# Kernel optimization log

Hardware: AMD Instinct MI355X
Metric: run time of the kernel (lower is better)

## Reference

```python
import jax, jax.numpy as jnp
import numpy as np

N_NODES = 40000
N_EDGES = 640000
D = 128
D_OUT = 128


def _layernorm(x, gamma, beta, eps=1e-5):
    mu = jnp.mean(x, axis=-1, keepdims=True)
    var = jnp.mean(jnp.square(x - mu), axis=-1, keepdims=True)
    return (x - mu) * jax.lax.rsqrt(var + eps) * gamma + beta


def setup_inputs() -> dict:
    key = jax.random.key(0)
    ks = jax.random.split(key, 6)
    x = jax.random.normal(ks[0], (N_NODES, D), dtype=jnp.float32)
    edge_index = jax.random.randint(ks[1], (2, N_EDGES), 0, N_NODES, dtype=jnp.int64)
    s = 1.0 / np.sqrt(D)
    return {
        "x": x,
        "edge_index": edge_index,
        "ln1_w": jnp.ones((D,), jnp.float32),
        "ln1_b": jnp.zeros((D,), jnp.float32),
        "ln2_w": jnp.ones((D,), jnp.float32),
        "ln2_b": jnp.zeros((D,), jnp.float32),
        "w": jnp.ones((D,), jnp.float32),
        "W1": jax.random.normal(ks[2], (D, D), jnp.float32) * s,
        "W2": jax.random.normal(ks[3], (D, D), jnp.float32) * s,
        "O1": jax.random.normal(ks[4], (2 * D, D), jnp.float32) * s,
        "O2": jax.random.normal(ks[5], (D, D_OUT), jnp.float32) * s,
    }


def reference(x, edge_index, ln1_w, ln1_b, ln2_w, ln2_b, w, W1, W2, O1, O2):
    row, col = edge_index[0], edge_index[1]
    n = x.shape[0]
    # gather + 2-layer message MLP (bias-free): [E, D]
    msg = jnp.maximum(x[row] @ W1, 0.0) @ W2
    # scatter_mean over destination nodes (zero where no incoming edges)
    agg = jax.ops.segment_sum(msg, col, num_segments=n)
    cnt = jax.ops.segment_sum(jnp.ones((msg.shape[0],), x.dtype), col, num_segments=n)
    agg = agg / jnp.maximum(cnt, 1.0)[:, None]
    agg_n = _layernorm(agg, ln1_w, ln1_b)
    # repulsion + residual + LayerNorm
    fx = _layernorm(x + (x - agg_n) * w, ln2_w, ln2_b)
    # concat + output MLP
    cat = jnp.concatenate([fx, agg_n], axis=1)
    return jnp.maximum(cat @ O1, 0.0) @ O2
```

## Files before the change

### kernel.cpp

```cpp
#include <hip/hip_runtime.h>
#include <hip/hip_bf16.h>

#define NN 40000
#define NE 640000
#define DD 128
#define CAP 64

typedef __attribute__((ext_vector_type(8))) short bf16x8;
typedef __attribute__((ext_vector_type(8))) unsigned short u16x8;
typedef __attribute__((ext_vector_type(4))) float f32x4;

__device__ __forceinline__ unsigned short f2bf(float f) {
    __hip_bfloat16 h = __float2bfloat16(f);
    return *reinterpret_cast<unsigned short*>(&h);
}
__device__ __forceinline__ float bf2f(unsigned short u) {
    union { unsigned int ui; float f; } v;
    v.ui = ((unsigned int)u) << 16;
    return v.f;
}

__global__ __launch_bounds__(256) void prep_w_kernel(
    const float* __restrict__ W1, const float* __restrict__ W2,
    const float* __restrict__ O1, const float* __restrict__ O2,
    unsigned short* __restrict__ w1t, unsigned short* __restrict__ w2t,
    unsigned short* __restrict__ o1t, unsigned short* __restrict__ o2t)
{
    int t = blockIdx.x * 256 + threadIdx.x;
    if (t < 16384) {
        int n = t >> 7, k = t & 127;
        w1t[t] = f2bf(W1[k * 128 + n]);
    } else if (t < 32768) {
        int i = t - 16384;
        int n = i >> 7, k = i & 127;
        w2t[i] = f2bf(W2[k * 128 + n]);
    } else if (t < 65536) {
        int i = t - 32768;
        int n = i >> 8, k = i & 255;
        o1t[i] = f2bf(O1[k * 128 + n]);
    } else {
        int i = t - 65536;
        int n = i >> 7, k = i & 127;
        o2t[i] = f2bf(O2[k * 128 + n]);
    }
}

__global__ __launch_bounds__(256) void mlp1_kernel(
    const float* __restrict__ x, const unsigned short* __restrict__ w1t,
    const unsigned short* __restrict__ w2t, unsigned short* __restrict__ nm)
{
    __shared__ unsigned short xt[64 * 128];
    __shared__ unsigned short wb[128 * 128];
    __shared__ unsigned short hb[64 * 128];
    const int tid = threadIdx.x;
    const int row0 = blockIdx.x * 64;

    #pragma unroll
    for (int it = 0; it < 4; ++it) {
        int c = tid + it * 256;
        int r = c >> 4;
        int c0 = (c & 15) << 3;
        const float4* gp = reinterpret_cast<const float4*>(x + (size_t)(row0 + r) * DD + c0);
        float4 f0 = gp[0], f1 = gp[1];
        u16x8 p;
        p[0] = f2bf(f0.x); p[1] = f2bf(f0.y); p[2] = f2bf(f0.z); p[3] = f2bf(f0.w);
        p[4] = f2bf(f1.x); p[5] = f2bf(f1.y); p[6] = f2bf(f1.z); p[7] = f2bf(f1.w);
        unsigned b = (unsigned)((r * DD + c0) * 2) ^ ((unsigned)(r & 7) << 4);
        *reinterpret_cast<u16x8*>(reinterpret_cast<char*>(xt) + b) = p;
    }
    #pragma unroll
    for (int it = 0; it < 8; ++it) {
        int c = tid + it * 256;
        int n = c >> 4;
        int k0 = (c & 15) << 3;
        u16x8 v = *reinterpret_cast<const u16x8*>(w1t + n * DD + k0);
        unsigned b = (unsigned)((n * DD + k0) * 2) ^ ((unsigned)(n & 7) << 4);
        *reinterpret_cast<u16x8*>(reinterpret_cast<char*>(wb) + b) = v;
    }
    __syncthreads();

    const int lane = tid & 63;
    const int wv = tid >> 6;
    const int l15 = lane & 15;
    const int lg = lane >> 4;

    f32x4 acc[8];
    #pragma unroll
    for (int i = 0; i < 8; ++i) acc[i] = (f32x4){0.f, 0.f, 0.f, 0.f};

    #pragma unroll
    for (int kk = 0; kk < 4; ++kk) {
        int k = kk * 32 + lg * 8;
        int ar = wv * 16 + l15;
        bf16x8 a = *reinterpret_cast<const bf16x8*>(
            reinterpret_cast<const char*>(xt) + ((unsigned)((ar * DD + k) * 2) ^ ((unsigned)(ar & 7) << 4)));
        #pragma unroll
        for (int n0 = 0; n0 < 8; ++n0) {
            int bn = n0 * 16 + l15;
            bf16x8 bf = *reinterpret_cast<const bf16x8*>(
                reinterpret_cast<const char*>(wb) + ((unsigned)((bn * DD + k) * 2) ^ ((unsigned)(bn & 7) << 4)));
            acc[n0] = __builtin_amdgcn_mfma_f32_16x16x32_bf16(a, bf, acc[n0], 0, 0, 0);
        }
    }

    #pragma unroll
    for (int n0 = 0; n0 < 8; ++n0) {
        #pragma unroll
        for (int ri = 0; ri < 4; ++ri) {
            int r = wv * 16 + lg * 4 + ri;
            int cc = n0 * 16 + l15;
            float v = fmaxf(acc[n0][ri], 0.0f);
            *reinterpret_cast<unsigned short*>(
                reinterpret_cast<char*>(hb) + ((unsigned)((r * DD + cc) * 2) ^ ((unsigned)(r & 7) << 4))) = f2bf(v);
        }
    }
    __syncthreads();
    #pragma unroll
    for (int it = 0; it < 8; ++it) {
        int c = tid + it * 256;
        int n = c >> 4;
        int k0 = (c & 15) << 3;
        u16x8 v = *reinterpret_cast<const u16x8*>(w2t + n * DD + k0);
        unsigned b = (unsigned)((n * DD + k0) * 2) ^ ((unsigned)(n & 7) << 4);
        *reinterpret_cast<u16x8*>(reinterpret_cast<char*>(wb) + b) = v;
    }
    __syncthreads();

    f32x4 acc2[8];
    #pragma unroll
    for (int i = 0; i < 8; ++i) acc2[i] = (f32x4){0.f, 0.f, 0.f, 0.f};
    #pragma unroll
    for (int kk = 0; kk < 4; ++kk) {
        int k = kk * 32 + lg * 8;
        int ar = wv * 16 + l15;
        bf16x8 a = *reinterpret_cast<const bf16x8*>(
            reinterpret_cast<const char*>(hb) + ((unsigned)((ar * DD + k) * 2) ^ ((unsigned)(ar & 7) << 4)));
        #pragma unroll
        for (int n0 = 0; n0 < 8; ++n0) {
            int bn = n0 * 16 + l15;
            bf16x8 bf = *reinterpret_cast<const bf16x8*>(
                reinterpret_cast<const char*>(wb) + ((unsigned)((bn * DD + k) * 2) ^ ((unsigned)(bn & 7) << 4)));
            acc2[n0] = __builtin_amdgcn_mfma_f32_16x16x32_bf16(a, bf, acc2[n0], 0, 0, 0);
        }
    }
    #pragma unroll
    for (int n0 = 0; n0 < 8; ++n0) {
        #pragma unroll
        for (int ri = 0; ri < 4; ++ri) {
            int r = row0 + wv * 16 + lg * 4 + ri;
            int cc = n0 * 16 + l15;
            nm[(size_t)r * DD + cc] = f2bf(acc2[n0][ri]);
        }
    }
}

__global__ __launch_bounds__(256) void fill_kernel(
    const int* __restrict__ ei, unsigned int* __restrict__ cnt,
    unsigned short* __restrict__ srcs)
{
    const int t = blockIdx.x * 256 + threadIdx.x;
    int s[4], d[4];
    #pragma unroll
    for (int j = 0; j < 4; ++j) {
        int e = t + j * 160000;
        s[j] = ei[e];
        d[j] = ei[NE + e];
    }
    unsigned int p[4];
    #pragma unroll
    for (int j = 0; j < 4; ++j) p[j] = atomicAdd(cnt + d[j], 1u);
    #pragma unroll
    for (int j = 0; j < 4; ++j)
        if (p[j] < CAP) srcs[(size_t)d[j] * CAP + p[j]] = (unsigned short)s[j];
}

__global__ __launch_bounds__(256) void pull_node_kernel(
    const unsigned short* __restrict__ nm, const unsigned short* __restrict__ srcs,
    const unsigned int* __restrict__ cnt,
    const float* __restrict__ x,
    const float* __restrict__ g1, const float* __restrict__ b1,
    const float* __restrict__ g2, const float* __restrict__ b2,
    const float* __restrict__ w, unsigned short* __restrict__ catb)
{
    const int lane = threadIdx.x & 63;
    const int wv = threadIdx.x >> 6;
    const int i = blockIdx.x * 4 + wv;
    const int d0 = lane * 2;

    const unsigned int degf = cnt[i];
    const int deg = (int)(degf < CAP ? degf : CAP);
    const unsigned short* sp = srcs + (size_t)i * CAP;

    float a0 = 0.f, a1 = 0.f;
    int e = 0;
    for (; e + 4 <= deg; e += 4) {
        int s0 = sp[e + 0], s1 = sp[e + 1], s2 = sp[e + 2], s3 = sp[e + 3];
        ushort2 m0 = *reinterpret_cast<const ushort2*>(nm + (size_t)s0 * DD + d0);
        ushort2 m1 = *reinterpret_cast<const ushort2*>(nm + (size_t)s1 * DD + d0);
        ushort2 m2 = *reinterpret_cast<const ushort2*>(nm + (size_t)s2 * DD + d0);
        ushort2 m3 = *reinterpret_cast<const ushort2*>(nm + (size_t)s3 * DD + d0);
        a0 += bf2f(m0.x) + bf2f(m1.x) + bf2f(m2.x) + bf2f(m3.x);
        a1 += bf2f(m0.y) + bf2f(m1.y) + bf2f(m2.y) + bf2f(m3.y);
    }
    for (; e < deg; ++e) {
        int s0 = sp[e];
        ushort2 m0 = *reinterpret_cast<const ushort2*>(nm + (size_t)s0 * DD + d0);
        a0 += bf2f(m0.x);
        a1 += bf2f(m0.y);
    }

    float inv = 1.0f / fmaxf((float)degf, 1.0f);
    a0 *= inv; a1 *= inv;

    float s = a0 + a1;
    #pragma unroll
    for (int o = 32; o > 0; o >>= 1) s += __shfl_xor(s, o, 64);
    float mu = s * (1.0f / 128.0f);
    float e0 = a0 - mu, e1 = a1 - mu;
    float q = e0 * e0 + e1 * e1;
    #pragma unroll
    for (int o = 32; o > 0; o >>= 1) q += __shfl_xor(q, o, 64);
    float rs = rsqrtf(q * (1.0f / 128.0f) + 1e-5f);

    float2 g1v = *reinterpret_cast<const float2*>(g1 + d0);
    float2 b1v = *reinterpret_cast<const float2*>(b1 + d0);
    float an0 = e0 * rs * g1v.x + b1v.x;
    float an1 = e1 * rs * g1v.y + b1v.y;

    float2 xv = *reinterpret_cast<const float2*>(x + (size_t)i * DD + d0);
    float2 wv2 = *reinterpret_cast<const float2*>(w + d0);
    float t0 = xv.x + (xv.x - an0) * wv2.x;
    float t1 = xv.y + (xv.y - an1) * wv2.y;

    float s2 = t0 + t1;
    #pragma unroll
    for (int o = 32; o > 0; o >>= 1) s2 += __shfl_xor(s2, o, 64);
    float mu2 = s2 * (1.0f / 128.0f);
    float f0 = t0 - mu2, f1 = t1 - mu2;
    float q2 = f0 * f0 + f1 * f1;
    #pragma unroll
    for (int o = 32; o > 0; o >>= 1) q2 += __shfl_xor(q2, o, 64);
    float rs2 = rsqrtf(q2 * (1.0f / 128.0f) + 1e-5f);

    float2 g2v = *reinterpret_cast<const float2*>(g2 + d0);
    float2 b2v = *reinterpret_cast<const float2*>(b2 + d0);
    float fx0 = f0 * rs2 * g2v.x + b2v.x;
    float fx1 = f1 * rs2 * g2v.y + b2v.y;

    ushort2 uo; uo.x = f2bf(fx0); uo.y = f2bf(fx1);
    *reinterpret_cast<ushort2*>(catb + (size_t)i * 256 + d0) = uo;
    ushort2 ua; ua.x = f2bf(an0); ua.y = f2bf(an1);
    *reinterpret_cast<ushort2*>(catb + (size_t)i * 256 + 128 + d0) = ua;
}

__global__ __launch_bounds__(256) void mlp2_kernel(
    const unsigned short* __restrict__ catb, const unsigned short* __restrict__ o1t,
    const unsigned short* __restrict__ o2t, float* __restrict__ out)
{
    __shared__ unsigned short ct[64 * 256];
    __shared__ unsigned short wb[128 * 128];
    unsigned short* hb = ct;
    const int tid = threadIdx.x;
    const int row0 = blockIdx.x * 64;

    #pragma unroll
    for (int it = 0; it < 8; ++it) {
        int c = tid + it * 256;
        int r = c >> 5;
        int c0 = (c & 31) << 3;
        u16x8 v = *reinterpret_cast<const u16x8*>(catb + (size_t)(row0 + r) * 256 + c0);
        unsigned b = (unsigned)((r * 256 + c0) * 2) ^ ((unsigned)(r & 7) << 4);
        *reinterpret_cast<u16x8*>(reinterpret_cast<char*>(ct) + b) = v;
    }

    const int lane = tid & 63;
    const int wv = tid >> 6;
    const int l15 = lane & 15;
    const int lg = lane >> 4;

    f32x4 acc[8];
    #pragma unroll
    for (int i = 0; i < 8; ++i) acc[i] = (f32x4){0.f, 0.f, 0.f, 0.f};

    for (int h = 0; h < 2; ++h) {
        #pragma unroll
        for (int it = 0; it < 8; ++it) {
            int c = tid + it * 256;
            int n = c >> 4;
            int k0 = (c & 15) << 3;
            u16x8 v = *reinterpret_cast<const u16x8*>(o1t + n * 256 + h * 128 + k0);
            unsigned b = (unsigned)((n * DD + k0) * 2) ^ ((unsigned)(n & 7) << 4);
            *reinterpret_cast<u16x8*>(reinterpret_cast<char*>(wb) + b) = v;
        }
        __syncthreads();
        #pragma unroll
        for (int kk = 0; kk < 4; ++kk) {
            int k = kk * 32 + lg * 8;
            int ar = wv * 16 + l15;
            bf16x8 a = *reinterpret_cast<const bf16x8*>(
                reinterpret_cast<const char*>(ct) +
                ((unsigned)((ar * 256 + h * 128 + k) * 2) ^ ((unsigned)(ar & 7) << 4)));
            #pragma unroll
            for (int n0 = 0; n0 < 8; ++n0) {
                int bn = n0 * 16 + l15;
                bf16x8 bf = *reinterpret_cast<const bf16x8*>(
                    reinterpret_cast<const char*>(wb) + ((unsigned)((bn * DD + k) * 2) ^ ((unsigned)(bn & 7) << 4)));
                acc[n0] = __builtin_amdgcn_mfma_f32_16x16x32_bf16(a, bf, acc[n0], 0, 0, 0);
            }
        }
        __syncthreads();
    }

    #pragma unroll
    for (int n0 = 0; n0 < 8; ++n0) {
        #pragma unroll
        for (int ri = 0; ri < 4; ++ri) {
            int r = wv * 16 + lg * 4 + ri;
            int cc = n0 * 16 + l15;
            float v = fmaxf(acc[n0][ri], 0.0f);
            *reinterpret_cast<unsigned short*>(
                reinterpret_cast<char*>(hb) + ((unsigned)((r * DD + cc) * 2) ^ ((unsigned)(r & 7) << 4))) = f2bf(v);
        }
    }
    #pragma unroll
    for (int it = 0; it < 8; ++it) {
        int c = tid + it * 256;
        int n = c >> 4;
        int k0 = (c & 15) << 3;
        u16x8 v = *reinterpret_cast<const u16x8*>(o2t + n * DD + k0);
        unsigned b = (unsigned)((n * DD + k0) * 2) ^ ((unsigned)(n & 7) << 4);
        *reinterpret_cast<u16x8*>(reinterpret_cast<char*>(wb) + b) = v;
    }
    __syncthreads();

    f32x4 acc2[8];
    #pragma unroll
    for (int i = 0; i < 8; ++i) acc2[i] = (f32x4){0.f, 0.f, 0.f, 0.f};
    #pragma unroll
    for (int kk = 0; kk < 4; ++kk) {
        int k = kk * 32 + lg * 8;
        int ar = wv * 16 + l15;
        bf16x8 a = *reinterpret_cast<const bf16x8*>(
            reinterpret_cast<const char*>(hb) + ((unsigned)((ar * DD + k) * 2) ^ ((unsigned)(ar & 7) << 4)));
        #pragma unroll
        for (int n0 = 0; n0 < 8; ++n0) {
            int bn = n0 * 16 + l15;
            bf16x8 bf = *reinterpret_cast<const bf16x8*>(
                reinterpret_cast<const char*>(wb) + ((unsigned)((bn * DD + k) * 2) ^ ((unsigned)(bn & 7) << 4)));
            acc2[n0] = __builtin_amdgcn_mfma_f32_16x16x32_bf16(a, bf, acc2[n0], 0, 0, 0);
        }
    }

    #pragma unroll
    for (int n0 = 0; n0 < 8; ++n0) {
        #pragma unroll
        for (int ri = 0; ri < 4; ++ri) {
            int r = row0 + wv * 16 + lg * 4 + ri;
            int cc = n0 * 16 + l15;
            out[(size_t)r * DD + cc] = acc2[n0][ri];
        }
    }
}

extern "C" void kernel_launch(void* const* d_in, const int* in_sizes, int n_in,
                              void* d_out, int out_size, void* d_ws, size_t ws_size,
                              hipStream_t stream) {
    const float* x   = (const float*)d_in[0];
    const int*   ei  = (const int*)d_in[1];
    const float* g1  = (const float*)d_in[2];
    const float* b1  = (const float*)d_in[3];
    const float* g2  = (const float*)d_in[4];
    const float* b2  = (const float*)d_in[5];
    const float* w   = (const float*)d_in[6];
    const float* W1  = (const float*)d_in[7];
    const float* W2  = (const float*)d_in[8];
    const float* O1  = (const float*)d_in[9];
    const float* O2  = (const float*)d_in[10];
    float* out = (float*)d_out;

    char* ws = (char*)d_ws;
    unsigned short* nm   = (unsigned short*)(ws);
    unsigned short* catb = (unsigned short*)(ws + 10240000);
    unsigned short* srcs = (unsigned short*)(ws + 30720000);
    unsigned int*   cnt  = (unsigned int*)(ws + 35840000);
    unsigned short* w1t  = (unsigned short*)(ws + 36000000);
    unsigned short* w2t  = (unsigned short*)(ws + 36032768);
    unsigned short* o1t  = (unsigned short*)(ws + 36065536);
    unsigned short* o2t  = (unsigned short*)(ws + 36131072);

    prep_w_kernel<<<320, 256, 0, stream>>>(W1, W2, O1, O2, w1t, w2t, o1t, o2t);
    hipMemsetAsync(cnt, 0, (size_t)NN * 4, stream);
    mlp1_kernel<<<NN / 64, 256, 0, stream>>>(x, w1t, w2t, nm);
    fill_kernel<<<625, 256, 0, stream>>>(ei, cnt, srcs);
    pull_node_kernel<<<NN / 4, 256, 0, stream>>>(nm, srcs, cnt, x, g1, b1, g2, b2, w, catb);
    mlp2_kernel<<<NN / 64, 256, 0, stream>>>(catb, o1t, o2t, out);
}
```

Baseline: 182.2 us.

## Fuse edge fill into MLP1 launch, fold memset into prep, shrink LDS

Counter zeroing moves into the weight-prep kernel, replacing a separate memset. The edge-bucketing fill becomes extra blocks of the first MLP kernel so both run concurrently. Each fill block scans an 8000-edge chunk and handles only destinations in its node slice, which localizes atomics but makes every edge be read 8 times. The MLP kernels also reuse or halve their LDS buffers to raise occupancy, and the gather loop is unrolled by 8 for more memory-level parallelism.

```diff
diff --git a/kernel.cpp b/kernel.cpp
--- a/kernel.cpp
+++ b/kernel.cpp
@@ -5,6 +5,9 @@
 #define NE 640000
 #define DD 128
 #define CAP 64
+#define SLICE 5000
+#define FILLB 640
+#define FCHUNK 8000
 
 typedef __attribute__((ext_vector_type(8))) short bf16x8;
 typedef __attribute__((ext_vector_type(8))) unsigned short u16x8;
@@ -20,13 +23,20 @@
     return v.f;
 }
 
-__global__ __launch_bounds__(256) void prep_w_kernel(
+__global__ __launch_bounds__(256) void prep_kernel(
     const float* __restrict__ W1, const float* __restrict__ W2,
     const float* __restrict__ O1, const float* __restrict__ O2,
     unsigned short* __restrict__ w1t, unsigned short* __restrict__ w2t,
-    unsigned short* __restrict__ o1t, unsigned short* __restrict__ o2t)
+    unsigned short* __restrict__ o1t, unsigned short* __restrict__ o2t,
+    unsigned int* __restrict__ cnt)
 {
-    int t = blockIdx.x * 256 + threadIdx.x;
+    int bx = blockIdx.x;
+    if (bx >= 320) {
+        int t = (bx - 320) * 256 + threadIdx.x;
+        if (t < NN) cnt[t] = 0u;
+        return;
+    }
+    int t = bx * 256 + threadIdx.x;
     if (t < 16384) {
         int n = t >> 7, k = t & 127;
         w1t[t] = f2bf(W1[k * 128 + n]);
@@ -45,15 +55,35 @@
     }
 }
 
-__global__ __launch_bounds__(256) void mlp1_kernel(
+__global__ __launch_bounds__(256) void mega1_kernel(
     const float* __restrict__ x, const unsigned short* __restrict__ w1t,
-    const unsigned short* __restrict__ w2t, unsigned short* __restrict__ nm)
+    const unsigned short* __restrict__ w2t, unsigned short* __restrict__ nm,
+    const int* __restrict__ ei, unsigned int* __restrict__ cnt,
+    unsigned short* __restrict__ srcs)
 {
     __shared__ unsigned short xt[64 * 128];
     __shared__ unsigned short wb[128 * 128];
-    __shared__ unsigned short hb[64 * 128];
     const int tid = threadIdx.x;
-    const int row0 = blockIdx.x * 64;
+    const int bx = blockIdx.x;
+
+    if (bx >= 625) {
+        const int fb = bx - 625;
+        const int slice = bx & 7;
+        const int rank = fb >> 3;
+        const int base = rank * FCHUNK;
+        for (int j = tid; j < FCHUNK; j += 256) {
+            int e = base + j;
+            int d = ei[NE + e];
+            int s = ei[e];
+            if ((unsigned)d / SLICE == (unsigned)slice) {
+                unsigned int p = atomicAdd(cnt + d, 1u);
+                if (p < CAP) srcs[(size_t)d * CAP + p] = (unsigned short)s;
+            }
+        }
+        return;
+    }
+
+    const int row0 = bx * 64;
 
     #pragma unroll
     for (int it = 0; it < 4; ++it) {
@@ -102,7 +132,9 @@
             acc[n0] = __builtin_amdgcn_mfma_f32_16x16x32_bf16(a, bf, acc[n0], 0, 0, 0);
         }
     }
-
+    __syncthreads();
+
+    unsigned short* hb = xt;
     #pragma unroll
     for (int n0 = 0; n0 < 8; ++n0) {
         #pragma unroll
@@ -114,7 +146,6 @@
                 reinterpret_cast<char*>(hb) + ((unsigned)((r * DD + cc) * 2) ^ ((unsigned)(r & 7) << 4))) = f2bf(v);
         }
     }
-    __syncthreads();
     #pragma unroll
     for (int it = 0; it < 8; ++it) {
         int c = tid + it * 256;
@@ -152,26 +183,6 @@
             nm[(size_t)r * DD + cc] = f2bf(acc2[n0][ri]);
         }
     }
-}
-
-__global__ __launch_bounds__(256) void fill_kernel(
-    const int* __restrict__ ei, unsigned int* __restrict__ cnt,
-    unsigned short* __restrict__ srcs)
-{
-    const int t = blockIdx.x * 256 + threadIdx.x;
-    int s[4], d[4];
-    #pragma unroll
-    for (int j = 0; j < 4; ++j) {
-        int e = t + j * 160000;
-        s[j] = ei[e];
-        d[j] = ei[NE + e];
-    }
-    unsigned int p[4];
-    #pragma unroll
-    for (int j = 0; j < 4; ++j) p[j] = atomicAdd(cnt + d[j], 1u);
-    #pragma unroll
-    for (int j = 0; j < 4; ++j)
-        if (p[j] < CAP) srcs[(size_t)d[j] * CAP + p[j]] = (unsigned short)s[j];
 }
 
 __global__ __launch_bounds__(256) void pull_node_kernel(
@@ -193,6 +204,17 @@
 
     float a0 = 0.f, a1 = 0.f;
     int e = 0;
+    for (; e + 8 <= deg; e += 8) {
+        int s[8];
+        #pragma unroll
+        for (int j = 0; j < 8; ++j) s[j] = sp[e + j];
+        ushort2 m[8];
+        #pragma unroll
+        for (int j = 0; j < 8; ++j)
+            m[j] = *reinterpret_cast<const ushort2*>(nm + (size_t)s[j] * DD + d0);
+        #pragma unroll
+        for (int j = 0; j < 8; ++j) { a0 += bf2f(m[j].x); a1 += bf2f(m[j].y); }
+    }
     for (; e + 4 <= deg; e += 4) {
         int s0 = sp[e + 0], s1 = sp[e + 1], s2 = sp[e + 2], s3 = sp[e + 3];
         ushort2 m0 = *reinterpret_cast<const ushort2*>(nm + (size_t)s0 * DD + d0);
@@ -257,22 +279,10 @@
     const unsigned short* __restrict__ catb, const unsigned short* __restrict__ o1t,
     const unsigned short* __restrict__ o2t, float* __restrict__ out)
 {
-    __shared__ unsigned short ct[64 * 256];
+    __shared__ unsigned short ct[64 * 128];
     __shared__ unsigned short wb[128 * 128];
-    unsigned short* hb = ct;
     const int tid = threadIdx.x;
     const int row0 = blockIdx.x * 64;
-
-    #pragma unroll
-    for (int it = 0; it < 8; ++it) {
-        int c = tid + it * 256;
-        int r = c >> 5;
-        int c0 = (c & 31) << 3;
-        u16x8 v = *reinterpret_cast<const u16x8*>(catb + (size_t)(row0 + r) * 256 + c0);
-        unsigned b = (unsigned)((r * 256 + c0) * 2) ^ ((unsigned)(r & 7) << 4);
-        *reinterpret_cast<u16x8*>(reinterpret_cast<char*>(ct) + b) = v;
-    }
-
     const int lane = tid & 63;
     const int wv = tid >> 6;
     const int l15 = lane & 15;
@@ -283,13 +293,22 @@
     for (int i = 0; i < 8; ++i) acc[i] = (f32x4){0.f, 0.f, 0.f, 0.f};
 
     for (int h = 0; h < 2; ++h) {
+        #pragma unroll
+        for (int it = 0; it < 4; ++it) {
+            int c = tid + it * 256;
+            int r = c >> 4;
+            int c0 = (c & 15) << 3;
+            u16x8 v = *reinterpret_cast<const u16x8*>(catb + (size_t)(row0 + r) * 256 + h * 128 + c0);
+            unsigned b = (unsigned)((r * 128 + c0) * 2) ^ ((unsigned)(r & 7) << 4);
+            *reinterpret_cast<u16x8*>(reinterpret_cast<char*>(ct) + b) = v;
+        }
         #pragma unroll
         for (int it = 0; it < 8; ++it) {
             int c = tid + it * 256;
             int n = c >> 4;
             int k0 = (c & 15) << 3;
             u16x8 v = *reinterpret_cast<const u16x8*>(o1t + n * 256 + h * 128 + k0);
-            unsigned b = (unsigned)((n * DD + k0) * 2) ^ ((unsigned)(n & 7) << 4);
+            unsigned b = (unsigned)((n * 128 + k0) * 2) ^ ((unsigned)(n & 7) << 4);
             *reinterpret_cast<u16x8*>(reinterpret_cast<char*>(wb) + b) = v;
         }
         __syncthreads();
@@ -298,19 +317,19 @@
             int k = kk * 32 + lg * 8;
             int ar = wv * 16 + l15;
             bf16x8 a = *reinterpret_cast<const bf16x8*>(
-                reinterpret_cast<const char*>(ct) +
-                ((unsigned)((ar * 256 + h * 128 + k) * 2) ^ ((unsigned)(ar & 7) << 4)));
+                reinterpret_cast<const char*>(ct) + ((unsigned)((ar * 128 + k) * 2) ^ ((unsigned)(ar & 7) << 4)));
             #pragma unroll
             for (int n0 = 0; n0 < 8; ++n0) {
                 int bn = n0 * 16 + l15;
                 bf16x8 bf = *reinterpret_cast<const bf16x8*>(
-                    reinterpret_cast<const char*>(wb) + ((unsigned)((bn * DD + k) * 2) ^ ((unsigned)(bn & 7) << 4)));
+                    reinterpret_cast<const char*>(wb) + ((unsigned)((bn * 128 + k) * 2) ^ ((unsigned)(bn & 7) << 4)));
                 acc[n0] = __builtin_amdgcn_mfma_f32_16x16x32_bf16(a, bf, acc[n0], 0, 0, 0);
             }
         }
         __syncthreads();
     }
 
+    unsigned short* hb = ct;
     #pragma unroll
     for (int n0 = 0; n0 < 8; ++n0) {
         #pragma unroll
@@ -388,10 +407,8 @@
     unsigned short* o1t  = (unsigned short*)(ws + 36065536);
     unsigned short* o2t  = (unsigned short*)(ws + 36131072);
 
-    prep_w_kernel<<<320, 256, 0, stream>>>(W1, W2, O1, O2, w1t, w2t, o1t, o2t);
-    hipMemsetAsync(cnt, 0, (size_t)NN * 4, stream);
-    mlp1_kernel<<<NN / 64, 256, 0, stream>>>(x, w1t, w2t, nm);
-    fill_kernel<<<625, 256, 0, stream>>>(ei, cnt, srcs);
+    prep_kernel<<<477, 256, 0, stream>>>(W1, W2, O1, O2, w1t, w2t, o1t, o2t, cnt);
+    mega1_kernel<<<625 + FILLB, 256, 0, stream>>>(x, w1t, w2t, nm, ei, cnt, srcs);
     pull_node_kernel<<<NN / 4, 256, 0, stream>>>(nm, srcs, cnt, x, g1, b1, g2, b2, w, catb);
     mlp2_kernel<<<NN / 64, 256, 0, stream>>>(catb, o1t, o2t, out);
 }
```

Result: faster. 175.3 us (-3.8%).
